# Kernel tuning notes

Measured on AMD Instinct MI355X. Metric: run time of the kernel, lower is better.

The kernel has to match this reference:

```python
import jax, jax.numpy as jnp
import numpy as np
from jax.scipy.special import gammaln

N_I = 100000
N_J = 100000
D = 8
S_I = 6000
S_J = 6000
NNZ = 500000
EPS = 1e-06


def setup_inputs() -> dict:
    key = jax.random.key(0)
    ks = jax.random.split(key, 9)
    beta = jax.random.normal(ks[0], (N_I,), dtype=jnp.float32)
    gamma = jax.random.normal(ks[1], (N_J,), dtype=jnp.float32)
    latent_zi = jax.random.normal(ks[2], (N_I, D), dtype=jnp.float32)
    latent_zj = jax.random.normal(ks[3], (N_J, D), dtype=jnp.float32)
    # multinomial-without-replacement node samples -> random permutation prefix
    sample_i_idx = jax.random.permutation(ks[4], N_I)[:S_I]
    sample_j_idx = jax.random.permutation(ks[5], N_J)[:S_J]
    # spspmm-selected subgraph links (global node indices) with edge counts
    sparse_i_sample = jax.random.randint(ks[6], (NNZ,), 0, N_I)
    sparse_j_sample = jax.random.randint(ks[7], (NNZ,), 0, N_J)
    valueC = jax.random.uniform(ks[8], (NNZ,), dtype=jnp.float32)
    return {
        'beta': beta, 'gamma': gamma,
        'latent_zi': latent_zi, 'latent_zj': latent_zj,
        'valueC': valueC,
        'sample_i_idx': sample_i_idx, 'sample_j_idx': sample_j_idx,
        'sparse_i_sample': sparse_i_sample, 'sparse_j_sample': sparse_j_sample,
    }


def reference(beta, gamma, latent_zi, latent_zj, valueC,
              sample_i_idx, sample_j_idx, sparse_i_sample, sparse_j_sample):
    # Dense non-link term over sampled (I, J) block
    zi = latent_zi[sample_i_idx]            # [S_I, D]
    zj = latent_zj[sample_j_idx]            # [S_J, D]
    diff = zi[:, None, :] - zj[None, :, :] + EPS   # [S_I, S_J, D]
    z_dist = jnp.sqrt(jnp.sum(diff * diff, axis=-1))  # [S_I, S_J]
    Lambda = beta[sample_i_idx][:, None] + gamma[sample_j_idx][None, :] - z_dist
    # Sparse link terms (Poisson log-likelihood)
    dl = latent_zi[sparse_i_sample] - latent_zj[sparse_j_sample] + EPS  # [NNZ, D]
    z_dist_links = jnp.sqrt(jnp.sum(dl * dl, axis=-1))                  # [NNZ]
    bias_links = beta[sparse_i_sample] + gamma[sparse_j_sample]
    log_Lambda_links = valueC * (bias_links - z_dist_links)
    LL = jnp.sum(log_Lambda_links - gammaln(valueC + 1.0)) - jnp.sum(jnp.exp(Lambda))
    return LL
```

## Files before the change

### kernel.cpp

```cpp
#include <hip/hip_runtime.h>
#include <math.h>

#define NI_TOT 100000
#define NJ_TOT 100000
#define DD 8
#define SI_N 6000
#define SJ_N 6000
#define NNZ_N 500000
#define EPSF 1e-6f
#define LOG2E 1.44269504088896f

#define TI 64
#define JPT 4
#define JTILE (256 * JPT)
#define ND_I ((SI_N + TI - 1) / TI)
#define NJT ((SJ_N + JTILE - 1) / JTILE)
#define N_DENSE_BLOCKS (ND_I * NJT)
#define SPARSE_BLOCK 256
#define N_SPARSE_BLOCKS ((NNZ_N + SPARSE_BLOCK - 1) / SPARSE_BLOCK)
#define N_TOTAL_BLOCKS (N_DENSE_BLOCKS + N_SPARSE_BLOCKS)

#define GA1 (-0.577191652f)
#define GA2 ( 0.988205891f)
#define GA3 (-0.897056937f)
#define GA4 ( 0.918206857f)
#define GA5 (-0.756704078f)
#define GA6 ( 0.482199394f)
#define GA7 (-0.193527818f)
#define GA8 ( 0.035868343f)

__device__ __forceinline__ float2 fma2(float2 a, float2 b, float2 c) {
    return make_float2(fmaf(a.x, b.x, c.x), fmaf(a.y, b.y, c.y));
}
__device__ __forceinline__ float2 add2(float2 a, float2 b) {
    return make_float2(a.x + b.x, a.y + b.y);
}
__device__ __forceinline__ float2 sub2(float2 a, float2 b) {
    return make_float2(a.x - b.x, a.y - b.y);
}
__device__ __forceinline__ float2 max2(float2 a, float b) {
    return make_float2(fmaxf(a.x, b), fmaxf(a.y, b));
}

__global__ __launch_bounds__(256, 2) void fused_kernel(
    const float* __restrict__ beta, const float* __restrict__ gamma,
    const float* __restrict__ zi_all, const float* __restrict__ zj_all,
    const float* __restrict__ valueC,
    const int* __restrict__ si, const int* __restrict__ sj,
    const int* __restrict__ spi, const int* __restrict__ spj,
    float* __restrict__ partials, float* __restrict__ out, int atomic_mode)
{
    __shared__ float sRed[4];
    const int t = threadIdx.x;

    float blocksum = 0.0f;

    if (blockIdx.x < N_DENSE_BLOCKS) {
        __shared__ __align__(16) float  sZi[TI * DD];
        __shared__ __align__(8)  float2 sIB[TI];

        const int it = blockIdx.x % ND_I;
        const int js = blockIdx.x / ND_I;
        const int i0 = it * TI;

        for (int idx = t; idx < TI * DD; idx += 256) {
            int r = idx >> 3, d = idx & 7;
            int gi = i0 + r;
            float v = (gi < SI_N) ? zi_all[(size_t)si[gi] * DD + d] : 0.0f;
            sZi[idx] = (v + EPSF) * LOG2E;
        }
        __syncthreads();
        if (t < TI) {
            int gi = i0 + t;
            float s = 0.0f;
#pragma unroll
            for (int d = 0; d < DD; ++d) {
                float v = sZi[t * DD + d];
                s = fmaf(v, v, s);
            }
            float bL = (gi < SI_N) ? beta[si[gi]] * LOG2E : -1e30f;
            sIB[t] = make_float2(s, bL);
        }

        const int jb = js * JTILE + t * JPT;
        float zjr[JPT][DD];
        float gl[JPT], s2[JPT];
#pragma unroll
        for (int p = 0; p < JPT; ++p) {
            int gj = jb + p;
            if (gj < SJ_N) {
                int row = sj[gj];
                const float4* q = (const float4*)(zj_all + (size_t)row * DD);
                float4 q0 = q[0], q1 = q[1];
                zjr[p][0] = q0.x * LOG2E; zjr[p][1] = q0.y * LOG2E;
                zjr[p][2] = q0.z * LOG2E; zjr[p][3] = q0.w * LOG2E;
                zjr[p][4] = q1.x * LOG2E; zjr[p][5] = q1.y * LOG2E;
                zjr[p][6] = q1.z * LOG2E; zjr[p][7] = q1.w * LOG2E;
                gl[p] = gamma[row] * LOG2E;
            } else {
#pragma unroll
                for (int d = 0; d < DD; ++d) zjr[p][d] = 0.0f;
                gl[p] = -1e30f;
            }
            float s = 0.0f;
#pragma unroll
            for (int d = 0; d < DD; ++d) s = fmaf(zjr[p][d], zjr[p][d], s);
            s2[p] = s;
        }
        float2 zj2[DD][2];
#pragma unroll
        for (int d = 0; d < DD; ++d) {
            zj2[d][0] = make_float2(zjr[0][d], zjr[1][d]);
            zj2[d][1] = make_float2(zjr[2][d], zjr[3][d]);
        }
        const float2 gjL2[2] = {make_float2(gl[0], gl[1]), make_float2(gl[2], gl[3])};
        const float2 sj22[2] = {make_float2(s2[0], s2[1]), make_float2(s2[2], s2[3])};

        __syncthreads();

        const float2 m2 = make_float2(-2.0f, -2.0f);
        float acc0 = 0.0f, acc1 = 0.0f;
        float4 cr0 = *(const float4*)&sZi[0];
        float4 cr1 = *(const float4*)&sZi[4];
        float2 cib = sIB[0];
#pragma unroll 4
        for (int a = 0; a < TI; ++a) {
            float4 nr0, nr1; float2 nib;
            if (a + 1 < TI) {
                nr0 = *(const float4*)&sZi[(a + 1) * DD];
                nr1 = *(const float4*)&sZi[(a + 1) * DD + 4];
                nib = sIB[a + 1];
            }
            const float za[DD] = {cr0.x, cr0.y, cr0.z, cr0.w,
                                  cr1.x, cr1.y, cr1.z, cr1.w};
            float2 dot0 = make_float2(0.f, 0.f), dot1 = make_float2(0.f, 0.f);
#pragma unroll
            for (int d = 0; d < DD; ++d) {
                const float2 zd = make_float2(za[d], za[d]);
                dot0 = fma2(zd, zj2[d][0], dot0);
                dot1 = fma2(zd, zj2[d][1], dot1);
            }
            const float2 cs2 = make_float2(cib.x, cib.x);
            float2 ss0 = fma2(dot0, m2, add2(cs2, sj22[0]));
            float2 ss1 = fma2(dot1, m2, add2(cs2, sj22[1]));
            ss0 = max2(ss0, 1e-20f);
            ss1 = max2(ss1, 1e-20f);
            const float2 bb = make_float2(cib.y, cib.y);
            const float2 bg0 = add2(bb, gjL2[0]);
            const float2 bg1 = add2(bb, gjL2[1]);
            float2 x0 = sub2(bg0, make_float2(__builtin_amdgcn_sqrtf(ss0.x),
                                              __builtin_amdgcn_sqrtf(ss0.y)));
            float2 x1 = sub2(bg1, make_float2(__builtin_amdgcn_sqrtf(ss1.x),
                                              __builtin_amdgcn_sqrtf(ss1.y)));
            acc0 += __builtin_amdgcn_exp2f(x0.x) + __builtin_amdgcn_exp2f(x1.x);
            acc1 += __builtin_amdgcn_exp2f(x0.y) + __builtin_amdgcn_exp2f(x1.y);
            cr0 = nr0; cr1 = nr1; cib = nib;
        }
        blocksum = -(acc0 + acc1);
    } else {
        const int idx = (blockIdx.x - N_DENSE_BLOCKS) * SPARSE_BLOCK + t;
        float val = 0.0f;
        if (idx < NNZ_N) {
            const int i = spi[idx], j = spj[idx];
            const float4* zi4 = (const float4*)(zi_all + (size_t)i * DD);
            const float4* zj4 = (const float4*)(zj_all + (size_t)j * DD);
            float4 a0 = zi4[0], a1 = zi4[1];
            float4 b0 = zj4[0], b1 = zj4[1];
            float ss = 0.0f, df;
            df = a0.x - b0.x + EPSF; ss = fmaf(df, df, ss);
            df = a0.y - b0.y + EPSF; ss = fmaf(df, df, ss);
            df = a0.z - b0.z + EPSF; ss = fmaf(df, df, ss);
            df = a0.w - b0.w + EPSF; ss = fmaf(df, df, ss);
            df = a1.x - b1.x + EPSF; ss = fmaf(df, df, ss);
            df = a1.y - b1.y + EPSF; ss = fmaf(df, df, ss);
            df = a1.z - b1.z + EPSF; ss = fmaf(df, df, ss);
            df = a1.w - b1.w + EPSF; ss = fmaf(df, df, ss);
            ss = fmaxf(ss, 1e-20f);
            const float dist = __builtin_amdgcn_sqrtf(ss);
            const float c = valueC[idx];
            float g = 1.0f + c*(GA1 + c*(GA2 + c*(GA3 + c*(GA4 + c*(GA5
                          + c*(GA6 + c*(GA7 + c*GA8)))))));
            val = c * (beta[i] + gamma[j] - dist)
                - __builtin_amdgcn_logf(g) * (1.0f / LOG2E);
        }
        blocksum = val;
    }

    float acc = blocksum;
#pragma unroll
    for (int off = 32; off; off >>= 1) acc += __shfl_down(acc, off, 64);
    const int lane = t & 63, w = t >> 6;
    if (lane == 0) sRed[w] = acc;
    __syncthreads();
    if (t == 0) {
        float s = sRed[0] + sRed[1] + sRed[2] + sRed[3];
        if (atomic_mode) atomicAdd(out, s);
        else partials[blockIdx.x] = s;
    }
}

__global__ __launch_bounds__(256) void final_reduce_kernel(
    const float* __restrict__ p, int n, float* __restrict__ out)
{
    __shared__ float sRed[4];
    float s0 = 0.0f, s1 = 0.0f, s2 = 0.0f, s3 = 0.0f;
    int i = threadIdx.x;
    for (; i + 768 < n; i += 1024) {
        s0 += p[i]; s1 += p[i + 256]; s2 += p[i + 512]; s3 += p[i + 768];
    }
    for (; i < n; i += 256) s0 += p[i];
    float s = (s0 + s1) + (s2 + s3);
#pragma unroll
    for (int off = 32; off; off >>= 1) s += __shfl_down(s, off, 64);
    const int lane = threadIdx.x & 63, w = threadIdx.x >> 6;
    if (lane == 0) sRed[w] = s;
    __syncthreads();
    if (threadIdx.x == 0) out[0] = sRed[0] + sRed[1] + sRed[2] + sRed[3];
}

extern "C" void kernel_launch(void* const* d_in, const int* in_sizes, int n_in,
                              void* d_out, int out_size, void* d_ws, size_t ws_size,
                              hipStream_t stream) {
    const float* beta   = (const float*)d_in[0];
    const float* gamma  = (const float*)d_in[1];
    const float* zi     = (const float*)d_in[2];
    const float* zj     = (const float*)d_in[3];
    const float* valueC = (const float*)d_in[4];
    const int* si   = (const int*)d_in[5];
    const int* sjx  = (const int*)d_in[6];
    const int* spi  = (const int*)d_in[7];
    const int* spj  = (const int*)d_in[8];
    float* out = (float*)d_out;

    const int ntot = N_TOTAL_BLOCKS;
    const size_t need = (size_t)ntot * sizeof(float);

    if (ws_size >= need) {
        float* p = (float*)d_ws;
        fused_kernel<<<ntot, 256, 0, stream>>>(
            beta, gamma, zi, zj, valueC, si, sjx, spi, spj, p, out, 0);
        final_reduce_kernel<<<1, 256, 0, stream>>>(p, ntot, out);
    } else {
        hipMemsetAsync(out, 0, sizeof(float), stream);
        fused_kernel<<<ntot, 256, 0, stream>>>(
            beta, gamma, zi, zj, valueC, si, sjx, spi, spj, nullptr, out, 1);
    }
}
```

Before: 120.0 us.

## Pack latent rows to fp16 for sparse gathers; halve dense j-per-thread

Adds a pre-pass that converts all latent rows and the beta/gamma biases to fp16 in the workspace. The sparse link path then gathers one 16-byte row per endpoint instead of 32 bytes, and each thread handles two links. The dense tile drops from four j columns per thread to two and loses the min-occupancy launch bound, giving more blocks and fewer registers per thread. The pre-pass reads and writes the full 200k-row tables every call, which likely costs more than the sparse traffic it saves. It also lowers accuracy of the link term.

```diff
diff --git a/kernel.cpp b/kernel.cpp
--- a/kernel.cpp
+++ b/kernel.cpp
@@ -1,4 +1,5 @@
 #include <hip/hip_runtime.h>
+#include <hip/hip_fp16.h>
 #include <math.h>
 
 #define NI_TOT 100000
@@ -11,14 +12,20 @@
 #define LOG2E 1.44269504088896f
 
 #define TI 64
-#define JPT 4
+#define JPT 2
 #define JTILE (256 * JPT)
 #define ND_I ((SI_N + TI - 1) / TI)
 #define NJT ((SJ_N + JTILE - 1) / JTILE)
 #define N_DENSE_BLOCKS (ND_I * NJT)
-#define SPARSE_BLOCK 256
-#define N_SPARSE_BLOCKS ((NNZ_N + SPARSE_BLOCK - 1) / SPARSE_BLOCK)
+#define LPT 2
+#define SPARSE_SPAN (256 * LPT)
+#define N_SPARSE_BLOCKS ((NNZ_N + SPARSE_SPAN - 1) / SPARSE_SPAN)
 #define N_TOTAL_BLOCKS (N_DENSE_BLOCKS + N_SPARSE_BLOCKS)
+
+#define NROWS (NI_TOT + NJ_TOT)
+#define HZ_BYTES ((size_t)NROWS * DD * 2)
+#define HB_BYTES ((size_t)NROWS * 2)
+#define PARTIALS_OFF (HZ_BYTES + HB_BYTES)
 
 #define GA1 (-0.577191652f)
 #define GA2 ( 0.988205891f)
@@ -29,26 +36,48 @@
 #define GA7 (-0.193527818f)
 #define GA8 ( 0.035868343f)
 
-__device__ __forceinline__ float2 fma2(float2 a, float2 b, float2 c) {
-    return make_float2(fmaf(a.x, b.x, c.x), fmaf(a.y, b.y, c.y));
-}
-__device__ __forceinline__ float2 add2(float2 a, float2 b) {
-    return make_float2(a.x + b.x, a.y + b.y);
-}
-__device__ __forceinline__ float2 sub2(float2 a, float2 b) {
-    return make_float2(a.x - b.x, a.y - b.y);
-}
-__device__ __forceinline__ float2 max2(float2 a, float b) {
-    return make_float2(fmaxf(a.x, b), fmaxf(a.y, b));
-}
-
-__global__ __launch_bounds__(256, 2) void fused_kernel(
+__global__ __launch_bounds__(256) void pack_kernel(
+    const float* __restrict__ beta, const float* __restrict__ gamma,
+    const float* __restrict__ zi_all, const float* __restrict__ zj_all,
+    __half* __restrict__ hz, __half* __restrict__ hb)
+{
+    const int r = blockIdx.x * 256 + threadIdx.x;
+    if (r < NROWS) {
+        const float* src = (r < NI_TOT) ? zi_all + (size_t)r * DD
+                                        : zj_all + (size_t)(r - NI_TOT) * DD;
+        float4 a = ((const float4*)src)[0];
+        float4 b = ((const float4*)src)[1];
+        __half2 h0 = __floats2half2_rn(a.x, a.y);
+        __half2 h1 = __floats2half2_rn(a.z, a.w);
+        __half2 h2 = __floats2half2_rn(b.x, b.y);
+        __half2 h3 = __floats2half2_rn(b.z, b.w);
+        uint4 u;
+        u.x = *(unsigned*)&h0; u.y = *(unsigned*)&h1;
+        u.z = *(unsigned*)&h2; u.w = *(unsigned*)&h3;
+        ((uint4*)hz)[r] = u;
+    } else if (r < 2 * NROWS) {
+        const int q = r - NROWS;
+        float v = (q < NI_TOT) ? beta[q] : gamma[q - NI_TOT];
+        hb[q] = __float2half(v);
+    }
+}
+
+__device__ __forceinline__ void unpack_row(uint4 u, float f[DD]) {
+    float2 p;
+    p = __half22float2(*(__half2*)&u.x); f[0] = p.x; f[1] = p.y;
+    p = __half22float2(*(__half2*)&u.y); f[2] = p.x; f[3] = p.y;
+    p = __half22float2(*(__half2*)&u.z); f[4] = p.x; f[5] = p.y;
+    p = __half22float2(*(__half2*)&u.w); f[6] = p.x; f[7] = p.y;
+}
+
+__global__ __launch_bounds__(256) void fused_kernel(
     const float* __restrict__ beta, const float* __restrict__ gamma,
     const float* __restrict__ zi_all, const float* __restrict__ zj_all,
     const float* __restrict__ valueC,
     const int* __restrict__ si, const int* __restrict__ sj,
     const int* __restrict__ spi, const int* __restrict__ spj,
-    float* __restrict__ partials, float* __restrict__ out, int atomic_mode)
+    const __half* __restrict__ hz, const __half* __restrict__ hb,
+    float* __restrict__ partials, float* __restrict__ out, int mode)
 {
     __shared__ float sRed[4];
     const int t = threadIdx.x;
@@ -83,42 +112,44 @@
         }
 
         const int jb = js * JTILE + t * JPT;
-        float zjr[JPT][DD];
-        float gl[JPT], s2[JPT];
-#pragma unroll
-        for (int p = 0; p < JPT; ++p) {
-            int gj = jb + p;
+        float zA[DD], zB[DD], glA, glB, s2A, s2B;
+        {
+            int gj = jb;
             if (gj < SJ_N) {
                 int row = sj[gj];
                 const float4* q = (const float4*)(zj_all + (size_t)row * DD);
                 float4 q0 = q[0], q1 = q[1];
-                zjr[p][0] = q0.x * LOG2E; zjr[p][1] = q0.y * LOG2E;
-                zjr[p][2] = q0.z * LOG2E; zjr[p][3] = q0.w * LOG2E;
-                zjr[p][4] = q1.x * LOG2E; zjr[p][5] = q1.y * LOG2E;
-                zjr[p][6] = q1.z * LOG2E; zjr[p][7] = q1.w * LOG2E;
-                gl[p] = gamma[row] * LOG2E;
+                zA[0]=q0.x*LOG2E; zA[1]=q0.y*LOG2E; zA[2]=q0.z*LOG2E; zA[3]=q0.w*LOG2E;
+                zA[4]=q1.x*LOG2E; zA[5]=q1.y*LOG2E; zA[6]=q1.z*LOG2E; zA[7]=q1.w*LOG2E;
+                glA = gamma[row] * LOG2E;
             } else {
 #pragma unroll
-                for (int d = 0; d < DD; ++d) zjr[p][d] = 0.0f;
-                gl[p] = -1e30f;
-            }
-            float s = 0.0f;
-#pragma unroll
-            for (int d = 0; d < DD; ++d) s = fmaf(zjr[p][d], zjr[p][d], s);
-            s2[p] = s;
-        }
-        float2 zj2[DD][2];
-#pragma unroll
-        for (int d = 0; d < DD; ++d) {
-            zj2[d][0] = make_float2(zjr[0][d], zjr[1][d]);
-            zj2[d][1] = make_float2(zjr[2][d], zjr[3][d]);
-        }
-        const float2 gjL2[2] = {make_float2(gl[0], gl[1]), make_float2(gl[2], gl[3])};
-        const float2 sj22[2] = {make_float2(s2[0], s2[1]), make_float2(s2[2], s2[3])};
-
+                for (int d = 0; d < DD; ++d) zA[d] = 0.0f;
+                glA = -1e30f;
+            }
+            gj = jb + 1;
+            if (gj < SJ_N) {
+                int row = sj[gj];
+                const float4* q = (const float4*)(zj_all + (size_t)row * DD);
+                float4 q0 = q[0], q1 = q[1];
+                zB[0]=q0.x*LOG2E; zB[1]=q0.y*LOG2E; zB[2]=q0.z*LOG2E; zB[3]=q0.w*LOG2E;
+                zB[4]=q1.x*LOG2E; zB[5]=q1.y*LOG2E; zB[6]=q1.z*LOG2E; zB[7]=q1.w*LOG2E;
+                glB = gamma[row] * LOG2E;
+            } else {
+#pragma unroll
+                for (int d = 0; d < DD; ++d) zB[d] = 0.0f;
+                glB = -1e30f;
+            }
+            float sa = 0.0f, sb = 0.0f;
+#pragma unroll
+            for (int d = 0; d < DD; ++d) {
+                sa = fmaf(zA[d], zA[d], sa);
+                sb = fmaf(zB[d], zB[d], sb);
+            }
+            s2A = sa; s2B = sb;
+        }
         __syncthreads();
 
-        const float2 m2 = make_float2(-2.0f, -2.0f);
         float acc0 = 0.0f, acc1 = 0.0f;
         float4 cr0 = *(const float4*)&sZi[0];
         float4 cr1 = *(const float4*)&sZi[4];
@@ -131,57 +162,73 @@
                 nr1 = *(const float4*)&sZi[(a + 1) * DD + 4];
                 nib = sIB[a + 1];
             }
-            const float za[DD] = {cr0.x, cr0.y, cr0.z, cr0.w,
-                                  cr1.x, cr1.y, cr1.z, cr1.w};
-            float2 dot0 = make_float2(0.f, 0.f), dot1 = make_float2(0.f, 0.f);
-#pragma unroll
-            for (int d = 0; d < DD; ++d) {
-                const float2 zd = make_float2(za[d], za[d]);
-                dot0 = fma2(zd, zj2[d][0], dot0);
-                dot1 = fma2(zd, zj2[d][1], dot1);
-            }
-            const float2 cs2 = make_float2(cib.x, cib.x);
-            float2 ss0 = fma2(dot0, m2, add2(cs2, sj22[0]));
-            float2 ss1 = fma2(dot1, m2, add2(cs2, sj22[1]));
-            ss0 = max2(ss0, 1e-20f);
-            ss1 = max2(ss1, 1e-20f);
-            const float2 bb = make_float2(cib.y, cib.y);
-            const float2 bg0 = add2(bb, gjL2[0]);
-            const float2 bg1 = add2(bb, gjL2[1]);
-            float2 x0 = sub2(bg0, make_float2(__builtin_amdgcn_sqrtf(ss0.x),
-                                              __builtin_amdgcn_sqrtf(ss0.y)));
-            float2 x1 = sub2(bg1, make_float2(__builtin_amdgcn_sqrtf(ss1.x),
-                                              __builtin_amdgcn_sqrtf(ss1.y)));
-            acc0 += __builtin_amdgcn_exp2f(x0.x) + __builtin_amdgcn_exp2f(x1.x);
-            acc1 += __builtin_amdgcn_exp2f(x0.y) + __builtin_amdgcn_exp2f(x1.y);
+            float dA = 0.0f, dB = 0.0f;
+            dA = fmaf(cr0.x, zA[0], dA); dB = fmaf(cr0.x, zB[0], dB);
+            dA = fmaf(cr0.y, zA[1], dA); dB = fmaf(cr0.y, zB[1], dB);
+            dA = fmaf(cr0.z, zA[2], dA); dB = fmaf(cr0.z, zB[2], dB);
+            dA = fmaf(cr0.w, zA[3], dA); dB = fmaf(cr0.w, zB[3], dB);
+            dA = fmaf(cr1.x, zA[4], dA); dB = fmaf(cr1.x, zB[4], dB);
+            dA = fmaf(cr1.y, zA[5], dA); dB = fmaf(cr1.y, zB[5], dB);
+            dA = fmaf(cr1.z, zA[6], dA); dB = fmaf(cr1.z, zB[6], dB);
+            dA = fmaf(cr1.w, zA[7], dA); dB = fmaf(cr1.w, zB[7], dB);
+            float ssA = fmaf(dA, -2.0f, cib.x + s2A);
+            float ssB = fmaf(dB, -2.0f, cib.x + s2B);
+            ssA = fmaxf(ssA, 1e-20f);
+            ssB = fmaxf(ssB, 1e-20f);
+            float xA = cib.y + glA - __builtin_amdgcn_sqrtf(ssA);
+            float xB = cib.y + glB - __builtin_amdgcn_sqrtf(ssB);
+            acc0 += __builtin_amdgcn_exp2f(xA);
+            acc1 += __builtin_amdgcn_exp2f(xB);
             cr0 = nr0; cr1 = nr1; cib = nib;
         }
         blocksum = -(acc0 + acc1);
     } else {
-        const int idx = (blockIdx.x - N_DENSE_BLOCKS) * SPARSE_BLOCK + t;
+        const int base = (blockIdx.x - N_DENSE_BLOCKS) * SPARSE_SPAN + t;
         float val = 0.0f;
-        if (idx < NNZ_N) {
+        const uint4* hzv = (const uint4*)hz;
+#pragma unroll
+        for (int u = 0; u < LPT; ++u) {
+            const int idx = base + u * 256;
+            if (idx >= NNZ_N) continue;
             const int i = spi[idx], j = spj[idx];
-            const float4* zi4 = (const float4*)(zi_all + (size_t)i * DD);
-            const float4* zj4 = (const float4*)(zj_all + (size_t)j * DD);
-            float4 a0 = zi4[0], a1 = zi4[1];
-            float4 b0 = zj4[0], b1 = zj4[1];
-            float ss = 0.0f, df;
-            df = a0.x - b0.x + EPSF; ss = fmaf(df, df, ss);
-            df = a0.y - b0.y + EPSF; ss = fmaf(df, df, ss);
-            df = a0.z - b0.z + EPSF; ss = fmaf(df, df, ss);
-            df = a0.w - b0.w + EPSF; ss = fmaf(df, df, ss);
-            df = a1.x - b1.x + EPSF; ss = fmaf(df, df, ss);
-            df = a1.y - b1.y + EPSF; ss = fmaf(df, df, ss);
-            df = a1.z - b1.z + EPSF; ss = fmaf(df, df, ss);
-            df = a1.w - b1.w + EPSF; ss = fmaf(df, df, ss);
-            ss = fmaxf(ss, 1e-20f);
-            const float dist = __builtin_amdgcn_sqrtf(ss);
             const float c = valueC[idx];
+            float dist, bg;
+            if (mode == 0) {
+                uint4 ui = hzv[i];
+                uint4 uj = hzv[NI_TOT + j];
+                float fi[DD], fj[DD];
+                unpack_row(ui, fi);
+                unpack_row(uj, fj);
+                float ss = 0.0f;
+#pragma unroll
+                for (int d = 0; d < DD; ++d) {
+                    float df = fi[d] - fj[d] + EPSF;
+                    ss = fmaf(df, df, ss);
+                }
+                ss = fmaxf(ss, 1e-20f);
+                dist = __builtin_amdgcn_sqrtf(ss);
+                bg = __half2float(hb[i]) + __half2float(hb[NI_TOT + j]);
+            } else {
+                const float4* zi4 = (const float4*)(zi_all + (size_t)i * DD);
+                const float4* zj4 = (const float4*)(zj_all + (size_t)j * DD);
+                float4 a0 = zi4[0], a1 = zi4[1];
+                float4 b0 = zj4[0], b1 = zj4[1];
+                float ss = 0.0f, df;
+                df = a0.x-b0.x+EPSF; ss = fmaf(df,df,ss);
+                df = a0.y-b0.y+EPSF; ss = fmaf(df,df,ss);
+                df = a0.z-b0.z+EPSF; ss = fmaf(df,df,ss);
+                df = a0.w-b0.w+EPSF; ss = fmaf(df,df,ss);
+                df = a1.x-b1.x+EPSF; ss = fmaf(df,df,ss);
+                df = a1.y-b1.y+EPSF; ss = fmaf(df,df,ss);
+                df = a1.z-b1.z+EPSF; ss = fmaf(df,df,ss);
+                df = a1.w-b1.w+EPSF; ss = fmaf(df,df,ss);
+                ss = fmaxf(ss, 1e-20f);
+                dist = __builtin_amdgcn_sqrtf(ss);
+                bg = beta[i] + gamma[j];
+            }
             float g = 1.0f + c*(GA1 + c*(GA2 + c*(GA3 + c*(GA4 + c*(GA5
                           + c*(GA6 + c*(GA7 + c*GA8)))))));
-            val = c * (beta[i] + gamma[j] - dist)
-                - __builtin_amdgcn_logf(g) * (1.0f / LOG2E);
+            val += c * (bg - dist) - __builtin_amdgcn_logf(g) * (1.0f / LOG2E);
         }
         blocksum = val;
     }
@@ -194,7 +241,7 @@
     __syncthreads();
     if (t == 0) {
         float s = sRed[0] + sRed[1] + sRed[2] + sRed[3];
-        if (atomic_mode) atomicAdd(out, s);
+        if (mode) atomicAdd(out, s);
         else partials[blockIdx.x] = s;
     }
 }
@@ -233,16 +280,21 @@
     float* out = (float*)d_out;
 
     const int ntot = N_TOTAL_BLOCKS;
-    const size_t need = (size_t)ntot * sizeof(float);
+    const size_t need = PARTIALS_OFF + (size_t)ntot * sizeof(float);
 
     if (ws_size >= need) {
-        float* p = (float*)d_ws;
+        __half* hz = (__half*)d_ws;
+        __half* hb = (__half*)((char*)d_ws + HZ_BYTES);
+        float* p = (float*)((char*)d_ws + PARTIALS_OFF);
+        const int packb = (2 * NROWS + 255) / 256;
+        pack_kernel<<<packb, 256, 0, stream>>>(beta, gamma, zi, zj, hz, hb);
         fused_kernel<<<ntot, 256, 0, stream>>>(
-            beta, gamma, zi, zj, valueC, si, sjx, spi, spj, p, out, 0);
+            beta, gamma, zi, zj, valueC, si, sjx, spi, spj, hz, hb, p, out, 0);
         final_reduce_kernel<<<1, 256, 0, stream>>>(p, ntot, out);
     } else {
         hipMemsetAsync(out, 0, sizeof(float), stream);
         fused_kernel<<<ntot, 256, 0, stream>>>(
-            beta, gamma, zi, zj, valueC, si, sjx, spi, spj, nullptr, out, 1);
-    }
-}
+            beta, gamma, zi, zj, valueC, si, sjx, spi, spj,
+            (const __half*)zi, (const __half*)zi, nullptr, out, 1);
+    }
+}
```

New measurement: 110.9 us. 1.08x faster.
